# Optimization experiments

Measured on AMD Instinct MI355X. Metric: run time of the kernel, lower is better.

## Reference

```python
import jax, jax.numpy as jnp
import numpy as np

N = 4096
IN_DIM = 512
NUM_HEADS = 8
SUB_DIM = 64
ETA = 0.5
LAMBDA_SPARSE = 0.1
EDGE_PROB = 0.01


def setup_inputs() -> dict:
    key = jax.random.key(0)
    k_h, k_u, k_a = jax.random.split(key, 3)
    H = jax.random.normal(k_h, (N, IN_DIM), dtype=jnp.float32)
    # Per-head orthonormal subspace bases (QR init, as in the torch module)
    raw = jax.random.normal(k_u, (NUM_HEADS, IN_DIM, SUB_DIM), dtype=jnp.float32)
    U = jax.vmap(lambda a: jnp.linalg.qr(a)[0])(raw)  # [K, in_dim, r]
    # Binary adjacency mask with self-loops (float 0/1)
    adj = (jax.random.uniform(k_a, (N, N)) < EDGE_PROB).astype(jnp.float32)
    adj_mask = jnp.maximum(adj, jnp.eye(N, dtype=jnp.float32))
    threshold = jnp.full((IN_DIM,), LAMBDA_SPARSE, dtype=jnp.float32)
    return {"H": H, "adj_mask": adj_mask, "U": U, "threshold": threshold}


def reference(H, adj_mask, U, threshold):
    r = U.shape[-1]
    scale = jnp.asarray(r, H.dtype) ** 0.5
    # Z_k = U_k^T H^T  -> [K, r, n]
    Z = jnp.einsum('kdr,nd->krn', U, H)
    # scores[k, i, j] = Z_k[:, i] . Z_k[:, j] / sqrt(r), masked to neighbors
    scores = jnp.einsum('kri,krj->kij', Z, Z) / scale
    scores = scores + (1.0 - adj_mask) * (-1e9)
    alpha = jax.nn.softmax(scores, axis=-1)          # [K, n, n]
    # Z_agg[k, :, i] = sum_j alpha[k, i, j] * Z_k[:, j]
    Z_agg = jnp.einsum('krj,kij->kri', Z, alpha)      # [K, r, n]
    # project back and sum heads: [n, d]
    agg = jnp.einsum('kdr,kri->id', U, Z_agg)
    H_half = H + ETA * agg
    H_out = jax.nn.relu(H_half - threshold[None, :])
    # orthogonality loss: sum_{k<l} ||U_k^T U_l||_F^2
    gram = jnp.einsum('kdr,lds->klrs', U, U)
    sq = jnp.sum(gram ** 2, axis=(-1, -2))            # [K, K]
    orth_loss = 0.5 * (jnp.sum(sq) - jnp.trace(sq))
    return H_out, orth_loss
```

## Files before the change

kernel.cpp:

```cpp
#include <hip/hip_runtime.h>
#include <hip/hip_bf16.h>

#define NN   4096
#define DD   512
#define KH   8
#define RR   64
#define CAP  128

typedef unsigned short u16;
typedef unsigned int   u32;
typedef unsigned long long u64;
typedef __attribute__((ext_vector_type(8))) short short8;
typedef __attribute__((ext_vector_type(4))) float f32x4;

__device__ __forceinline__ float bflo(u32 v){ union{u32 i; float f;} c; c.i = v << 16;        return c.f; }
__device__ __forceinline__ float bfhi(u32 v){ union{u32 i; float f;} c; c.i = v & 0xFFFF0000u; return c.f; }
__device__ __forceinline__ u16 f2bf(float f){ __hip_bfloat16 h = __float2bfloat16(f); return *reinterpret_cast<u16*>(&h); }

__global__ __launch_bounds__(256) void prep_scan(const float* __restrict__ H, const float* __restrict__ U,
                                                 u16* __restrict__ Hb, u16* __restrict__ Bt1,
                                                 u16* __restrict__ Bt2,
                                                 float* __restrict__ lossP) {
    union SH {
        float tile[64][65];
        struct { float UkT[32][20]; float UlT[32][68]; } o;
    };
    __shared__ SH sh;
    __shared__ float red4[4];
    const int b = blockIdx.x, t = threadIdx.x;

    if (b < 112) {
        const int ob = b;
        const int pb = ob >> 2, strip = ob & 3;
        int idx = pb, k = 0, lh = 1;
        #pragma unroll
        for (int kk = 0; kk < 8; kk++) {
            int c = 7 - kk;
            if (idx < c) { k = kk; lh = kk + 1 + idx; break; }
            idx -= c;
        }
        const int r = t & 15;
        const int s0 = (t >> 4) * 4;
        const int r0g = strip * 16;
        const float* Uk = U + (size_t)k  * DD * RR;
        const float* Ul = U + (size_t)lh * DD * RR;
        float a0 = 0.f, a1 = 0.f, a2 = 0.f, a3 = 0.f;
        for (int dc = 0; dc < DD; dc += 32) {
            if (t < 128) {
                int dd = t >> 2, rq = t & 3;
                *(float4*)&sh.o.UkT[dd][rq * 4] = *(const float4*)(Uk + (size_t)(dc + dd) * RR + r0g + rq * 4);
            }
            #pragma unroll
            for (int s = 0; s < 2; s++) {
                int u = t + 256 * s;
                int dd = u >> 4, sq = u & 15;
                *(float4*)&sh.o.UlT[dd][sq * 4] = *(const float4*)(Ul + (size_t)(dc + dd) * RR + sq * 4);
            }
            __syncthreads();
            #pragma unroll 4
            for (int dd = 0; dd < 32; dd++) {
                float a = sh.o.UkT[dd][r];
                float4 bv = *(const float4*)&sh.o.UlT[dd][s0];
                a0 += a * bv.x; a1 += a * bv.y; a2 += a * bv.z; a3 += a * bv.w;
            }
            __syncthreads();
        }
        float v = a0 * a0 + a1 * a1 + a2 * a2 + a3 * a3;
        #pragma unroll
        for (int off = 32; off; off >>= 1) v += __shfl_down(v, off, 64);
        if ((t & 63) == 0) red4[t >> 6] = v;
        __syncthreads();
        if (t == 0) lossP[ob] = red4[0] + red4[1] + red4[2] + red4[3];
        return;
    }
    if (b < 176) {
        const int b2 = b - 112;
        const int k = b2 >> 3, d0 = (b2 & 7) * 64;
        #pragma unroll
        for (int s = 0; s < 4; s++) {
            int u = t + 256 * s;
            int dd = u >> 4, rq = u & 15;
            float4 v = *(const float4*)(U + ((size_t)(k * DD + d0 + dd)) * RR + rq * 4);
            sh.tile[dd][rq * 4 + 0] = v.x; sh.tile[dd][rq * 4 + 1] = v.y;
            sh.tile[dd][rq * 4 + 2] = v.z; sh.tile[dd][rq * 4 + 3] = v.w;
        }
        __syncthreads();
        {   int r = t >> 2;
            #pragma unroll
            for (int ii = 0; ii < 16; ii++) {
                int dd = (t & 3) * 16 + ii;
                Bt1[(size_t)(k * RR + r) * DD + d0 + dd] = f2bf(sh.tile[dd][r]);
            }
        }
        {   int dd = t >> 2, rb = (t & 3) * 16;
            #pragma unroll
            for (int ii = 0; ii < 16; ii++) {
                Bt2[(size_t)(d0 + dd) * DD + k * RR + rb + ii] = f2bf(sh.tile[dd][rb + ii]);
            }
        }
        return;
    }
    const size_t id = (size_t)(b - 176) * 256 + t;
    float4 v = *(const float4*)(H + id * 4);
    ushort4 o; o.x = f2bf(v.x); o.y = f2bf(v.y); o.z = f2bf(v.z); o.w = f2bf(v.w);
    *(ushort4*)(Hb + id * 4) = o;
}

__global__ __launch_bounds__(256) void zgemm_scan(const u16* __restrict__ Hb, const u16* __restrict__ Bt1,
                                                  u16* __restrict__ Zb,
                                                  const float* __restrict__ adj,
                                                  int* __restrict__ nlist, int* __restrict__ cnt) {
    __shared__ short As[64][72];
    __shared__ short Bs[64][72];
    const int b = blockIdx.x, t = threadIdx.x;

    if (b % 3 != 2) {
        const int sg = (b / 3) * 2 + (b % 3);
        const int row = sg * 4 + (t >> 6);
        const int lane = t & 63;
        const float* arow = adj + (size_t)row * NN;
        int* ndst = nlist + (size_t)row * CAP;
        const u64 lt = (1ull << lane) - 1;
        int base = 0;
        #pragma unroll
        for (int h = 0; h < 2; h++) {
            float4 mv[8];
            #pragma unroll
            for (int c = 0; c < 8; c++)
                mv[c] = *(const float4*)(arow + (h * 8 + c) * 256 + lane * 4);
            #pragma unroll
            for (int c = 0; c < 8; c++) {
                const int j = (h * 8 + c) * 256 + lane * 4;
                const u64 bx = __ballot(mv[c].x != 0.f);
                const u64 by = __ballot(mv[c].y != 0.f);
                const u64 bz = __ballot(mv[c].z != 0.f);
                const u64 bw = __ballot(mv[c].w != 0.f);
                const int nx = __popcll(bx), ny = __popcll(by), nz = __popcll(bz);
                if (mv[c].x != 0.f) { int p = base + __popcll(bx & lt);                if (p < CAP) ndst[p] = j;     }
                if (mv[c].y != 0.f) { int p = base + nx + __popcll(by & lt);           if (p < CAP) ndst[p] = j + 1; }
                if (mv[c].z != 0.f) { int p = base + nx + ny + __popcll(bz & lt);      if (p < CAP) ndst[p] = j + 2; }
                if (mv[c].w != 0.f) { int p = base + nx + ny + nz + __popcll(bw & lt); if (p < CAP) ndst[p] = j + 3; }
                base += nx + ny + nz + __popcll(bw);
            }
        }
        if (lane == 0) cnt[row] = min(base, CAP);
        return;
    }

    const int g = b / 3;
    const int i0 = (g & 63) * 64, n0 = (g >> 6) * 64;
    const int w = t >> 6, lane = t & 63;
    const int lm = lane & 15, lg = lane >> 4;
    f32x4 acc[4] = {};
    for (int kc = 0; kc < DD; kc += 64) {
        #pragma unroll
        for (int s = 0; s < 2; s++) {
            int c = t + 256 * s; int row = c >> 3, gg = c & 7;
            *(short8*)&As[row][gg * 8] = *(const short8*)(Hb  + (size_t)(i0 + row) * DD + kc + gg * 8);
            *(short8*)&Bs[row][gg * 8] = *(const short8*)(Bt1 + (size_t)(n0 + row) * DD + kc + gg * 8);
        }
        __syncthreads();
        #pragma unroll
        for (int ks = 0; ks < 64; ks += 32) {
            short8 af = *(const short8*)&As[w * 16 + lm][ks + lg * 8];
            #pragma unroll
            for (int bb = 0; bb < 4; bb++) {
                short8 bfr = *(const short8*)&Bs[bb * 16 + lm][ks + lg * 8];
                acc[bb] = __builtin_amdgcn_mfma_f32_16x16x32_bf16(af, bfr, acc[bb], 0, 0, 0);
            }
        }
        __syncthreads();
    }
    #pragma unroll
    for (int bb = 0; bb < 4; bb++)
        #pragma unroll
        for (int q = 0; q < 4; q++) {
            int row = i0 + w * 16 + lg * 4 + q;
            int col = n0 + bb * 16 + lm;
            Zb[(size_t)row * DD + col] = f2bf(acc[bb][q]);
        }
}

__global__ __launch_bounds__(512) void attn11(const u16* __restrict__ Zb, const int* __restrict__ nlist,
                                              const int* __restrict__ cnt, u16* __restrict__ Zaggb) {
    const int i = blockIdx.x, t = threadIdx.x;
    const int w = t >> 6, lane = t & 63;
    __shared__ int   nbrS[CAP];
    __shared__ float red[KH][DD];
    __shared__ float lS[KH][KH + 1];
    const int ci = cnt[i];
    if (t < CAP) nbrS[t] = nlist[(size_t)i * CAP + min(t, ci - 1)];
    __syncthreads();

    float a[8];
    {
        uint4 av = *(const uint4*)(Zb + (size_t)i * DD + lane * 8);
        a[0] = bflo(av.x); a[1] = bfhi(av.x); a[2] = bflo(av.y); a[3] = bfhi(av.y);
        a[4] = bflo(av.z); a[5] = bfhi(av.z); a[6] = bflo(av.w); a[7] = bfhi(av.w);
    }

    float l = 0.f;
    float acc[8] = {};
    const int nIt = (ci + 7) >> 3;

    uint4 b0 = *(const uint4*)(Zb + (size_t)nbrS[min(w, ci - 1)] * DD + lane * 8);
    uint4 b1 = *(const uint4*)(Zb + (size_t)nbrS[min(w + 8, ci - 1)] * DD + lane * 8);

    #define PROCESS(c, val)                                                        \
    {   float zf[8];                                                               \
        zf[0] = bflo(c.x); zf[1] = bfhi(c.x); zf[2] = bflo(c.y); zf[3] = bfhi(c.y);\
        zf[4] = bflo(c.z); zf[5] = bfhi(c.z); zf[6] = bflo(c.w); zf[7] = bfhi(c.w);\
        float s = zf[0]*a[0] + zf[1]*a[1] + zf[2]*a[2] + zf[3]*a[3]                \
                + zf[4]*a[4] + zf[5]*a[5] + zf[6]*a[6] + zf[7]*a[7];               \
        s += __shfl_xor(s, 1); s += __shfl_xor(s, 2); s += __shfl_xor(s, 4);       \
        const float e = (val) ? __expf(s * 0.125f) : 0.f;                          \
        l += e;                                                                    \
        _Pragma("unroll")                                                          \
        for (int d = 0; d < 8; d++) acc[d] += e * zf[d];                           \
    }

    for (int tt = 0; tt < nIt; tt += 2) {
        {   const uint4 c = b0;
            const int pf = min(w + 8 * (tt + 2), ci - 1);
            b0 = *(const uint4*)(Zb + (size_t)nbrS[pf] * DD + lane * 8);
            const bool val = (w + 8 * tt) < ci;
            PROCESS(c, val);
        }
        if (tt + 1 < nIt) {
            const uint4 c = b1;
            const int pf = min(w + 8 * (tt + 3), ci - 1);
            b1 = *(const uint4*)(Zb + (size_t)nbrS[pf] * DD + lane * 8);
            const bool val = (w + 8 * (tt + 1)) < ci;
            PROCESS(c, val);
        }
    }
    #undef PROCESS

    *(float4*)&red[w][lane * 8]     = make_float4(acc[0], acc[1], acc[2], acc[3]);
    *(float4*)&red[w][lane * 8 + 4] = make_float4(acc[4], acc[5], acc[6], acc[7]);
    if ((lane & 7) == 0) lS[w][lane >> 3] = l;
    __syncthreads();

    const int d = t, k = d >> 6;
    float ls = 0.f, sum = 0.f;
    #pragma unroll
    for (int ww = 0; ww < KH; ww++) { ls += lS[ww][k]; sum += red[ww][d]; }
    Zaggb[(size_t)i * DD + d] = f2bf(sum / ls);
}

__global__ __launch_bounds__(256) void outgemm_mfma(const u16* __restrict__ Ab, const u16* __restrict__ Btb,
                                                    const float* __restrict__ H, const float* __restrict__ thr,
                                                    const float* __restrict__ lossP,
                                                    float* __restrict__ out) {
    __shared__ short As[64][72];
    __shared__ short Bs[64][72];
    const int t = threadIdx.x;
    const int i0 = blockIdx.x * 64, n0 = blockIdx.y * 64;
    if (i0 == 0 && n0 == 0 && t < 64) {
        float v = lossP[t] + ((t + 64 < 112) ? lossP[t + 64] : 0.f);
        #pragma unroll
        for (int off = 32; off; off >>= 1) v += __shfl_down(v, off, 64);
        if (t == 0) out[(size_t)NN * DD] = v;
    }
    const int w = t >> 6, lane = t & 63;
    const int lm = lane & 15, lg = lane >> 4;
    f32x4 acc[4] = {};
    for (int kc = 0; kc < DD; kc += 64) {
        #pragma unroll
        for (int s = 0; s < 2; s++) {
            int c = t + 256 * s; int row = c >> 3, g = c & 7;
            *(short8*)&As[row][g * 8] = *(const short8*)(Ab  + (size_t)(i0 + row) * DD + kc + g * 8);
            *(short8*)&Bs[row][g * 8] = *(const short8*)(Btb + (size_t)(n0 + row) * DD + kc + g * 8);
        }
        __syncthreads();
        #pragma unroll
        for (int ks = 0; ks < 64; ks += 32) {
            short8 af = *(const short8*)&As[w * 16 + lm][ks + lg * 8];
            #pragma unroll
            for (int b = 0; b < 4; b++) {
                short8 bfr = *(const short8*)&Bs[b * 16 + lm][ks + lg * 8];
                acc[b] = __builtin_amdgcn_mfma_f32_16x16x32_bf16(af, bfr, acc[b], 0, 0, 0);
            }
        }
        __syncthreads();
    }
    #pragma unroll
    for (int b = 0; b < 4; b++) {
        const int col = n0 + b * 16 + lm;
        const float th = thr[col];
        #pragma unroll
        for (int q = 0; q < 4; q++) {
            int row = i0 + w * 16 + lg * 4 + q;
            float h = H[(size_t)row * DD + col];
            out[(size_t)row * DD + col] = fmaxf(h + 0.5f * acc[b][q] - th, 0.f);
        }
    }
}

extern "C" void kernel_launch(void* const* d_in, const int* in_sizes, int n_in,
                              void* d_out, int out_size, void* d_ws, size_t ws_size,
                              hipStream_t stream) {
    const float* H   = (const float*)d_in[0];
    const float* adj = (const float*)d_in[1];
    const float* U   = (const float*)d_in[2];
    const float* thr = (const float*)d_in[3];
    float* out = (float*)d_out;

    char* ws = (char*)d_ws;
    float* lossP = (float*)ws;
    u16*   Hb    = (u16*)(ws + 1024);
    u16*   Zb    = (u16*)(ws + 1024 + 4u * 1024 * 1024);
    u16*   Zaggb = (u16*)(ws + 1024 + 8u * 1024 * 1024);
    u16*   Bt1   = (u16*)(ws + 1024 + 12u * 1024 * 1024);
    u16*   Bt2   = (u16*)(ws + 1024 + 12u * 1024 * 1024 + 512u * 1024);
    int*   nlist = (int*)(ws + 1024 + 13u * 1024 * 1024);
    int*   cnt   = (int*)(ws + 1024 + 15u * 1024 * 1024 + 512u * 1024);

    prep_scan<<<2224, 256, 0, stream>>>(H, U, Hb, Bt1, Bt2, lossP);
    zgemm_scan<<<1536, 256, 0, stream>>>(Hb, Bt1, Zb, adj, nlist, cnt);
    attn11<<<NN, 512, 0, stream>>>(Zb, nlist, cnt, Zaggb);
    outgemm_mfma<<<dim3(64, 8), 256, 0, stream>>>(Zaggb, Bt2, H, thr, lossP, out);
}
```

Measured before the change: 162.4 us.

## Merge prep and Z-GEMM/scan kernels, converting H and U to bf16 on the fly

Folds the prep kernel and the Z GEMM plus adjacency-scan kernel into one launch. The H to bf16 and U to Bt1 conversion buffers are dropped; the GEMM now loads fp32 H and U directly, converts them in registers and writes a transposed U tile into shared memory. This removes one kernel launch, a global round trip for Hb and Bt1, and a dependency barrier. The cost is redundant conversion work across tiles and scattered 2-byte transposed LDS stores that may cause bank conflicts.

```diff
diff --git a/kernel.cpp b/kernel.cpp
--- a/kernel.cpp
+++ b/kernel.cpp
@@ -17,11 +17,13 @@
 __device__ __forceinline__ float bfhi(u32 v){ union{u32 i; float f;} c; c.i = v & 0xFFFF0000u; return c.f; }
 __device__ __forceinline__ u16 f2bf(float f){ __hip_bfloat16 h = __float2bfloat16(f); return *reinterpret_cast<u16*>(&h); }
 
-__global__ __launch_bounds__(256) void prep_scan(const float* __restrict__ H, const float* __restrict__ U,
-                                                 u16* __restrict__ Hb, u16* __restrict__ Bt1,
-                                                 u16* __restrict__ Bt2,
-                                                 float* __restrict__ lossP) {
+__global__ __launch_bounds__(256) void k0_umbrella(const float* __restrict__ H, const float* __restrict__ U,
+                                                   const float* __restrict__ adj,
+                                                   u16* __restrict__ Bt2, u16* __restrict__ Zb,
+                                                   int* __restrict__ nlist, int* __restrict__ cnt,
+                                                   float* __restrict__ lossP) {
     union SH {
+        struct { short As[64][72]; short Bs[64][72]; } g;
         float tile[64][65];
         struct { float UkT[32][20]; float UlT[32][68]; } o;
     };
@@ -85,13 +87,6 @@
             sh.tile[dd][rq * 4 + 2] = v.z; sh.tile[dd][rq * 4 + 3] = v.w;
         }
         __syncthreads();
-        {   int r = t >> 2;
-            #pragma unroll
-            for (int ii = 0; ii < 16; ii++) {
-                int dd = (t & 3) * 16 + ii;
-                Bt1[(size_t)(k * RR + r) * DD + d0 + dd] = f2bf(sh.tile[dd][r]);
-            }
-        }
         {   int dd = t >> 2, rb = (t & 3) * 16;
             #pragma unroll
             for (int ii = 0; ii < 16; ii++) {
@@ -100,22 +95,9 @@
         }
         return;
     }
-    const size_t id = (size_t)(b - 176) * 256 + t;
-    float4 v = *(const float4*)(H + id * 4);
-    ushort4 o; o.x = f2bf(v.x); o.y = f2bf(v.y); o.z = f2bf(v.z); o.w = f2bf(v.w);
-    *(ushort4*)(Hb + id * 4) = o;
-}
-
-__global__ __launch_bounds__(256) void zgemm_scan(const u16* __restrict__ Hb, const u16* __restrict__ Bt1,
-                                                  u16* __restrict__ Zb,
-                                                  const float* __restrict__ adj,
-                                                  int* __restrict__ nlist, int* __restrict__ cnt) {
-    __shared__ short As[64][72];
-    __shared__ short Bs[64][72];
-    const int b = blockIdx.x, t = threadIdx.x;
-
-    if (b % 3 != 2) {
-        const int sg = (b / 3) * 2 + (b % 3);
+    const int u = b - 176;
+    if (u % 3 != 2) {
+        const int sg = (u / 3) * 2 + (u % 3);
         const int row = sg * 4 + (t >> 6);
         const int lane = t & 63;
         const float* arow = adj + (size_t)row * NN;
@@ -147,8 +129,9 @@
         return;
     }
 
-    const int g = b / 3;
+    const int g = u / 3;
     const int i0 = (g & 63) * 64, n0 = (g >> 6) * 64;
+    const int hk = g >> 6;
     const int w = t >> 6, lane = t & 63;
     const int lm = lane & 15, lg = lane >> 4;
     f32x4 acc[4] = {};
@@ -156,16 +139,37 @@
         #pragma unroll
         for (int s = 0; s < 2; s++) {
             int c = t + 256 * s; int row = c >> 3, gg = c & 7;
-            *(short8*)&As[row][gg * 8] = *(const short8*)(Hb  + (size_t)(i0 + row) * DD + kc + gg * 8);
-            *(short8*)&Bs[row][gg * 8] = *(const short8*)(Bt1 + (size_t)(n0 + row) * DD + kc + gg * 8);
+            const float* hp = H + (size_t)(i0 + row) * DD + kc + gg * 8;
+            float4 h0 = *(const float4*)hp, h1 = *(const float4*)(hp + 4);
+            short8 o;
+            o[0] = (short)f2bf(h0.x); o[1] = (short)f2bf(h0.y);
+            o[2] = (short)f2bf(h0.z); o[3] = (short)f2bf(h0.w);
+            o[4] = (short)f2bf(h1.x); o[5] = (short)f2bf(h1.y);
+            o[6] = (short)f2bf(h1.z); o[7] = (short)f2bf(h1.w);
+            *(short8*)&sh.g.As[row][gg * 8] = o;
+        }
+        {
+            int dd = t >> 2, rq = t & 3;
+            const float* up = U + ((size_t)(hk * DD) + kc + dd) * RR + rq * 16;
+            float4 u0 = *(const float4*)(up + 0), u1 = *(const float4*)(up + 4);
+            float4 u2 = *(const float4*)(up + 8), u3 = *(const float4*)(up + 12);
+            const int r0 = rq * 16;
+            sh.g.Bs[r0 +  0][dd] = (short)f2bf(u0.x); sh.g.Bs[r0 +  1][dd] = (short)f2bf(u0.y);
+            sh.g.Bs[r0 +  2][dd] = (short)f2bf(u0.z); sh.g.Bs[r0 +  3][dd] = (short)f2bf(u0.w);
+            sh.g.Bs[r0 +  4][dd] = (short)f2bf(u1.x); sh.g.Bs[r0 +  5][dd] = (short)f2bf(u1.y);
+            sh.g.Bs[r0 +  6][dd] = (short)f2bf(u1.z); sh.g.Bs[r0 +  7][dd] = (short)f2bf(u1.w);
+            sh.g.Bs[r0 +  8][dd] = (short)f2bf(u2.x); sh.g.Bs[r0 +  9][dd] = (short)f2bf(u2.y);
+            sh.g.Bs[r0 + 10][dd] = (short)f2bf(u2.z); sh.g.Bs[r0 + 11][dd] = (short)f2bf(u2.w);
+            sh.g.Bs[r0 + 12][dd] = (short)f2bf(u3.x); sh.g.Bs[r0 + 13][dd] = (short)f2bf(u3.y);
+            sh.g.Bs[r0 + 14][dd] = (short)f2bf(u3.z); sh.g.Bs[r0 + 15][dd] = (short)f2bf(u3.w);
         }
         __syncthreads();
         #pragma unroll
         for (int ks = 0; ks < 64; ks += 32) {
-            short8 af = *(const short8*)&As[w * 16 + lm][ks + lg * 8];
+            short8 af = *(const short8*)&sh.g.As[w * 16 + lm][ks + lg * 8];
             #pragma unroll
             for (int bb = 0; bb < 4; bb++) {
-                short8 bfr = *(const short8*)&Bs[bb * 16 + lm][ks + lg * 8];
+                short8 bfr = *(const short8*)&sh.g.Bs[bb * 16 + lm][ks + lg * 8];
                 acc[bb] = __builtin_amdgcn_mfma_f32_16x16x32_bf16(af, bfr, acc[bb], 0, 0, 0);
             }
         }
@@ -308,16 +312,13 @@
 
     char* ws = (char*)d_ws;
     float* lossP = (float*)ws;
-    u16*   Hb    = (u16*)(ws + 1024);
-    u16*   Zb    = (u16*)(ws + 1024 + 4u * 1024 * 1024);
-    u16*   Zaggb = (u16*)(ws + 1024 + 8u * 1024 * 1024);
-    u16*   Bt1   = (u16*)(ws + 1024 + 12u * 1024 * 1024);
-    u16*   Bt2   = (u16*)(ws + 1024 + 12u * 1024 * 1024 + 512u * 1024);
-    int*   nlist = (int*)(ws + 1024 + 13u * 1024 * 1024);
-    int*   cnt   = (int*)(ws + 1024 + 15u * 1024 * 1024 + 512u * 1024);
-
-    prep_scan<<<2224, 256, 0, stream>>>(H, U, Hb, Bt1, Bt2, lossP);
-    zgemm_scan<<<1536, 256, 0, stream>>>(Hb, Bt1, Zb, adj, nlist, cnt);
+    u16*   Zb    = (u16*)(ws + 1024);
+    u16*   Zaggb = (u16*)(ws + 1024 + 4u * 1024 * 1024);
+    u16*   Bt2   = (u16*)(ws + 1024 + 8u * 1024 * 1024);
+    int*   nlist = (int*)(ws + 1024 + 9u * 1024 * 1024);
+    int*   cnt   = (int*)(ws + 1024 + 11u * 1024 * 1024 + 512u * 1024);
+
+    k0_umbrella<<<1712, 256, 0, stream>>>(H, U, adj, Bt2, Zb, nlist, cnt, lossP);
     attn11<<<NN, 512, 0, stream>>>(Zb, nlist, cnt, Zaggb);
     outgemm_mfma<<<dim3(64, 8), 256, 0, stream>>>(Zaggb, Bt2, H, thr, lossP, out);
 }
```

New measurement: 158.1 us. -2.7%, faster.
